# Optimization experiments

Measured on AMD Instinct MI355X. Metric: run time of the kernel, lower is better.

Reference implementation:

```python
import jax, jax.numpy as jnp
import numpy as np

N_NODES = 50000


def setup_inputs() -> dict:
    key = jax.random.key(0)
    k1, k2, k3, k4, k5, k6 = jax.random.split(key, 6)
    c_in, c_out = 64, 64
    n_edges = 800000
    G = jax.random.normal(k1, (N_NODES, c_in), dtype=jnp.float32)
    RSC = jax.random.normal(k2, (N_NODES, c_in), dtype=jnp.float32)
    src = jax.random.randint(k3, (n_edges,), 0, N_NODES, dtype=jnp.int64)
    dst = jax.random.randint(k4, (n_edges,), 0, N_NODES, dtype=jnp.int64)
    W = jax.random.normal(k5, (c_out, c_in), dtype=jnp.float32) / np.sqrt(c_in)
    b = jax.random.normal(k6, (c_out,), dtype=jnp.float32) * 0.01
    return {"G": G, "RSC": RSC, "src": src, "dst": dst, "W": W, "b": b}


def reference(G, RSC, src, dst, W, b):
    # Per-edge relative feature: src node 'G' feature minus dst node 'RSC' feature
    rel = G[src] - RSC[dst]                          # [E, c_in]
    # Linear + ReLU (edge MLP)
    enc = jax.nn.relu(rel @ W.T + b)                 # [E, c_out]
    # Per-dst-node reductions over variable-size mailboxes
    max_agg = jax.ops.segment_max(enc, dst, num_segments=N_NODES)  # -inf for empty
    sum_agg = jax.ops.segment_sum(enc, dst, num_segments=N_NODES)
    cnt = jax.ops.segment_sum(jnp.ones_like(dst, dtype=enc.dtype), dst,
                              num_segments=N_NODES)               # [N]
    has_mail = (cnt > 0)[:, None]
    avg_agg = sum_agg / jnp.maximum(cnt, 1.0)[:, None]
    max_agg = jnp.where(has_mail, max_agg, 0.0)      # nodes w/o edges -> 0
    # concat(max, avg) as in reduce()
    return jnp.concatenate([max_agg, avg_agg], axis=-1)  # [N, 2*c_out]
```

## Files before the change

kernel.cpp:

```cpp
#include <hip/hip_runtime.h>
#include <hip/hip_bf16.h>

#define NCH 64
#define SPAN 64
#define HIST_BLOCKS 256
#define HIST_THREADS 1024
#define NBIN 256
#define NGEMM 768
#define FUSE_THREADS 512
#define NB_CAP 1536

__global__ void detect_init_kernel(const unsigned short* __restrict__ gp, int n16,
                                   const unsigned* __restrict__ ip, int niw,
                                   unsigned* __restrict__ flags,
                                   unsigned* __restrict__ gcnt, int nb) {
    if (blockIdx.x == 0) {
        __shared__ unsigned se, so;
        if (threadIdx.x == 0) { se = 0u; so = 0u; }
        __syncthreads();
        unsigned le = 0u, lo = 0u;
        for (int i = threadIdx.x; i < n16; i += blockDim.x) {
            unsigned ex = (unsigned)((gp[i] >> 7) & 0xFFu);
            if (ex >= 0xC0u) le++;
        }
        for (int i = threadIdx.x; i < niw; i += blockDim.x) {
            if ((i & 1) && ip[i] != 0u) lo++;
        }
        atomicAdd(&se, le);
        atomicAdd(&so, lo);
        __syncthreads();
        if (threadIdx.x == 0) {
            flags[0] = (se > 50u) ? 1u : 0u;
            flags[1] = (so < 50u) ? 1u : 0u;
        }
    } else {
        const int stride = (gridDim.x - 1) * blockDim.x;
        for (int i = (blockIdx.x - 1) * blockDim.x + threadIdx.x; i < nb; i += stride)
            gcnt[i] = 0u;
    }
}

__global__ void bucket_hist_kernel(const void* __restrict__ dstp,
                                   unsigned* __restrict__ gcnt,
                                   const unsigned* __restrict__ flags,
                                   int n_edges, int nb) {
    extern __shared__ unsigned lcnt[];
    for (int i = threadIdx.x; i < nb; i += blockDim.x) lcnt[i] = 0u;
    __syncthreads();
    const unsigned i64 = flags[1];
    const int stride = gridDim.x * blockDim.x;
    for (int e = blockIdx.x * blockDim.x + threadIdx.x; e < n_edges; e += stride) {
        int d = i64 ? (int)((const long long*)dstp)[e] : ((const int*)dstp)[e];
        atomicAdd(&lcnt[d >> 6], 1u);
    }
    __syncthreads();
    for (int i = threadIdx.x; i < nb; i += blockDim.x)
        if (lcnt[i]) atomicAdd(&gcnt[i], lcnt[i]);
}

__global__ void bucket_scan_kernel(const unsigned* __restrict__ gcnt,
                                   unsigned* __restrict__ boffs,
                                   unsigned* __restrict__ cursor, int nb) {
    __shared__ unsigned s[1024];
    const int t = threadIdx.x;
    const int L = (nb + 1023) / 1024;
    unsigned local = 0u;
    for (int i = 0; i < L; ++i) {
        int idx = t * L + i;
        if (idx < nb) local += gcnt[idx];
    }
    s[t] = local;
    __syncthreads();
    for (int off = 1; off < 1024; off <<= 1) {
        unsigned v = (t >= off) ? s[t - off] : 0u;
        __syncthreads();
        s[t] += v;
        __syncthreads();
    }
    unsigned run = s[t] - local;
    for (int i = 0; i < L; ++i) {
        int idx = t * L + i;
        if (idx < nb) { boffs[idx] = run; cursor[idx] = run; run += gcnt[idx]; }
    }
}

__global__ __launch_bounds__(FUSE_THREADS, 4)
void binning_gemm_kernel(const void* __restrict__ srcp, const void* __restrict__ dstp,
                         unsigned* __restrict__ cursor, unsigned* __restrict__ binned,
                         const unsigned* __restrict__ flags, int n_edges, int nb,
                         int depth,
                         const void* __restrict__ Gp, const void* __restrict__ Rp,
                         const void* __restrict__ Wp, const void* __restrict__ bp,
                         void* __restrict__ PQ, int n_nodes) {
    extern __shared__ unsigned lds[];
    if (blockIdx.x < NBIN) {
        unsigned* lcnt = lds;
        unsigned* stage = lds + nb;
        for (int i = threadIdx.x; i < nb; i += blockDim.x) lcnt[i] = 0u;
        __syncthreads();
        const unsigned i64 = flags[1];
        const int chunk = (n_edges + NBIN - 1) / NBIN;
        const int e0 = blockIdx.x * chunk;
        const int e1 = min(e0 + chunk, n_edges);
        for (int e = e0 + threadIdx.x; e < e1; e += blockDim.x) {
            int s, d;
            if (i64) {
                s = (int)((const long long*)srcp)[e];
                d = (int)((const long long*)dstp)[e];
            } else {
                s = ((const int*)srcp)[e];
                d = ((const int*)dstp)[e];
            }
            const int bkt = d >> 6;
            const unsigned pk = ((unsigned)(d & 63) << 26) | (unsigned)s;
            unsigned pos = atomicAdd(&lcnt[bkt], 1u);
            if ((int)pos < depth) {
                stage[bkt * depth + (int)pos] = pk;
            } else {
                unsigned g = atomicAdd(&cursor[bkt], 1u);
                binned[g] = pk;
            }
        }
        __syncthreads();
        for (int bkt = threadIdx.x; bkt < nb; bkt += blockDim.x) {
            int k = min((int)lcnt[bkt], depth);
            if (k > 0) {
                unsigned base = atomicAdd(&cursor[bkt], (unsigned)k);
                for (int i = 0; i < k; ++i) binned[base + i] = stage[bkt * depth + i];
            }
        }
    } else {
        const unsigned f32 = flags[0];
        const int lane = threadIdx.x & 63;
        const int waveInBlk = threadIdx.x >> 6;
        const int wavesPerBlk = blockDim.x >> 6;
        const int gwave = (blockIdx.x - NBIN) * wavesPerBlk + waveInBlk;
        const int nwaves = NGEMM * wavesPerBlk;
        const int n_rows = 2 * n_nodes;
        const int ngroups = (n_rows + 3) / 4;

        float* ldsb = (float*)lds;
        float* slot = &ldsb[waveInBlk * 4 * NCH];

        float w[NCH];
        float bias;
        if (f32) {
            const float* Wf = (const float*)Wp;
            #pragma unroll
            for (int k = 0; k < NCH; ++k) w[k] = Wf[lane * NCH + k];
            bias = ((const float*)bp)[lane];
        } else {
            const __hip_bfloat16* Wh = (const __hip_bfloat16*)Wp;
            #pragma unroll
            for (int k = 0; k < NCH; ++k) w[k] = __bfloat162float(Wh[lane * NCH + k]);
            bias = __bfloat162float(((const __hip_bfloat16*)bp)[lane]);
        }

        const int niter = (ngroups + nwaves - 1) / nwaves;
        for (int it = 0; it < niter; ++it) {
            const int grp = gwave + it * nwaves;
            const bool gvalid = (grp < ngroups);
            const int m0 = grp * 4;
            if (gvalid) {
                const int myrow = m0 + (lane >> 4);
                const int col = (lane & 15) * 4;
                float x0 = 0.f, x1 = 0.f, x2 = 0.f, x3 = 0.f;
                if (myrow < n_rows) {
                    const bool isQ = (myrow >= n_nodes);
                    const int r = isQ ? (myrow - n_nodes) : myrow;
                    const void* inp = isQ ? Rp : Gp;
                    if (f32) {
                        float4 v = *(const float4*)((const float*)inp +
                                                    (size_t)r * NCH + col);
                        x0 = v.x; x1 = v.y; x2 = v.z; x3 = v.w;
                    } else {
                        ushort4 v = *(const ushort4*)((const unsigned short*)inp +
                                                      (size_t)r * NCH + col);
                        x0 = __bfloat162float(*(__hip_bfloat16*)&v.x);
                        x1 = __bfloat162float(*(__hip_bfloat16*)&v.y);
                        x2 = __bfloat162float(*(__hip_bfloat16*)&v.z);
                        x3 = __bfloat162float(*(__hip_bfloat16*)&v.w);
                    }
                }
                const int sb = (lane >> 4) * NCH + col;
                slot[sb + 0] = x0; slot[sb + 1] = x1;
                slot[sb + 2] = x2; slot[sb + 3] = x3;
            }
            __syncthreads();
            if (gvalid) {
                #pragma unroll
                for (int rr = 0; rr < 4; ++rr) {
                    const int m = m0 + rr;
                    if (m < n_rows) {
                        float a0 = 0.f, a1 = 0.f, a2 = 0.f, a3 = 0.f;
                        const float4* r4 = (const float4*)(slot + rr * NCH);
                        #pragma unroll
                        for (int q = 0; q < 16; ++q) {
                            float4 rv = r4[q];
                            a0 = fmaf(rv.x, w[4 * q + 0], a0);
                            a1 = fmaf(rv.y, w[4 * q + 1], a1);
                            a2 = fmaf(rv.z, w[4 * q + 2], a2);
                            a3 = fmaf(rv.w, w[4 * q + 3], a3);
                        }
                        float acc = (a0 + a1) + (a2 + a3);
                        if (m >= n_nodes) acc -= bias;
                        if (f32) ((float*)PQ)[(size_t)m * NCH + lane] = acc;
                        else ((__hip_bfloat16*)PQ)[(size_t)m * NCH + lane] =
                                 __float2bfloat16(acc);
                    }
                }
            }
            __syncthreads();
        }
    }
}

__global__ __launch_bounds__(512)
void bucket_node_kernel(const unsigned* __restrict__ binned,
                        const unsigned* __restrict__ boffs,
                        const unsigned* __restrict__ gcnt,
                        const void* __restrict__ PQ,
                        const unsigned* __restrict__ flags,
                        void* __restrict__ outp, int n_nodes) {
    __shared__ unsigned scnt[SPAN];
    __shared__ unsigned soff[SPAN];
    __shared__ unsigned cur[SPAN];
    __shared__ unsigned dext[SPAN];
    __shared__ unsigned stage[NB_CAP];
    __shared__ unsigned sorted[NB_CAP];

    const int b = blockIdx.x;
    const int tid = threadIdx.x;
    const int estart = (int)boffs[b];
    const int count = (int)gcnt[b];
    const int lim = (count < NB_CAP) ? count : NB_CAP;

    if (tid < SPAN) { scnt[tid] = 0u; dext[tid] = 0u; }
    __syncthreads();

    for (int i = tid; i < count; i += 512) {
        const unsigned pk = binned[estart + i];
        if (i < NB_CAP) { stage[i] = pk; atomicAdd(&scnt[pk >> 26], 1u); }
        else atomicAdd(&dext[pk >> 26], 1u);
    }
    __syncthreads();

    if (tid == 0) {
        unsigned run = 0u;
        #pragma unroll
        for (int i = 0; i < SPAN; ++i) { soff[i] = run; cur[i] = run; run += scnt[i]; }
    }
    __syncthreads();

    for (int i = tid; i < lim; i += 512) {
        const unsigned pk = stage[i];
        const unsigned pos = atomicAdd(&cur[pk >> 26], 1u);
        sorted[pos] = pk & 0x03FFFFFFu;
    }
    __syncthreads();

    const unsigned f32 = flags[0];
    const int lane = tid & 63;
    const int wid = tid >> 6;
    const float* Pf = (const float*)PQ;
    const unsigned short* Ph = (const unsigned short*)PQ;

    for (int nn = wid; nn < SPAN; nn += 8) {
        const int n = b * SPAN + nn;
        if (n >= n_nodes) break;
        float q;
        if (f32) q = Pf[(size_t)(n_nodes + n) * NCH + lane];
        else {
            unsigned short h = Ph[(size_t)(n_nodes + n) * NCH + lane];
            q = __bfloat162float(*(__hip_bfloat16*)&h);
        }
        const int s0i = (int)soff[nn];
        const int scn = (int)scnt[nn];
        float vmax = 0.0f, vsum = 0.0f;
        int j = 0;
        for (; j + 4 <= scn; j += 4) {
            const int e0 = (int)sorted[s0i + j];
            const int e1 = (int)sorted[s0i + j + 1];
            const int e2 = (int)sorted[s0i + j + 2];
            const int e3 = (int)sorted[s0i + j + 3];
            float p0, p1, p2, p3;
            if (f32) {
                p0 = Pf[(size_t)e0 * NCH + lane];
                p1 = Pf[(size_t)e1 * NCH + lane];
                p2 = Pf[(size_t)e2 * NCH + lane];
                p3 = Pf[(size_t)e3 * NCH + lane];
            } else {
                unsigned short h0 = Ph[(size_t)e0 * NCH + lane];
                unsigned short h1 = Ph[(size_t)e1 * NCH + lane];
                unsigned short h2 = Ph[(size_t)e2 * NCH + lane];
                unsigned short h3 = Ph[(size_t)e3 * NCH + lane];
                p0 = __bfloat162float(*(__hip_bfloat16*)&h0);
                p1 = __bfloat162float(*(__hip_bfloat16*)&h1);
                p2 = __bfloat162float(*(__hip_bfloat16*)&h2);
                p3 = __bfloat162float(*(__hip_bfloat16*)&h3);
            }
            const float v0 = fmaxf(p0 - q, 0.0f);
            const float v1 = fmaxf(p1 - q, 0.0f);
            const float v2 = fmaxf(p2 - q, 0.0f);
            const float v3 = fmaxf(p3 - q, 0.0f);
            vmax = fmaxf(fmaxf(vmax, v0), fmaxf(v1, fmaxf(v2, v3)));
            vsum += (v0 + v1) + (v2 + v3);
        }
        for (; j < scn; ++j) {
            const int e = (int)sorted[s0i + j];
            float p;
            if (f32) p = Pf[(size_t)e * NCH + lane];
            else {
                unsigned short h = Ph[(size_t)e * NCH + lane];
                p = __bfloat162float(*(__hip_bfloat16*)&h);
            }
            const float v = fmaxf(p - q, 0.0f);
            vmax = fmaxf(vmax, v);
            vsum += v;
        }
        for (int i = NB_CAP; i < count; ++i) {
            const unsigned pk = binned[estart + i];
            if ((int)(pk >> 26) == nn) {
                const int e = (int)(pk & 0x03FFFFFFu);
                float p;
                if (f32) p = Pf[(size_t)e * NCH + lane];
                else {
                    unsigned short h = Ph[(size_t)e * NCH + lane];
                    p = __bfloat162float(*(__hip_bfloat16*)&h);
                }
                const float v = fmaxf(p - q, 0.0f);
                vmax = fmaxf(vmax, v);
                vsum += v;
            }
        }
        const int deg = scn + (int)dext[nn];
        const float avg = vsum / (float)(deg > 0 ? deg : 1);
        if (f32) {
            float* out = (float*)outp;
            out[(size_t)n * 2 * NCH + lane] = vmax;
            out[(size_t)n * 2 * NCH + NCH + lane] = avg;
        } else {
            __hip_bfloat16* out = (__hip_bfloat16*)outp;
            out[(size_t)n * 2 * NCH + lane] = __float2bfloat16(vmax);
            out[(size_t)n * 2 * NCH + NCH + lane] = __float2bfloat16(avg);
        }
    }
}

extern "C" void kernel_launch(void* const* d_in, const int* in_sizes, int n_in,
                              void* d_out, int out_size, void* d_ws, size_t ws_size,
                              hipStream_t stream) {
    const void* G = d_in[0];
    const void* RSC = d_in[1];
    const void* src = d_in[2];
    const void* dst = d_in[3];
    const void* W = d_in[4];
    const void* b = d_in[5];

    const int n_nodes = in_sizes[0] / NCH;
    const int n_edges = in_sizes[2];
    const int nb = (n_nodes + SPAN - 1) / SPAN;

    char* ws = (char*)d_ws;
    unsigned* flags = (unsigned*)ws;
    size_t off = 256;
    unsigned* binned = (unsigned*)(ws + off);
    off += (((size_t)n_edges * 4 + 255) / 256) * 256;
    unsigned* boffs = (unsigned*)(ws + off);
    off += (((size_t)nb * 4 + 255) / 256) * 256;
    unsigned* cursor = (unsigned*)(ws + off);
    off += (((size_t)nb * 4 + 255) / 256) * 256;
    unsigned* gcnt = (unsigned*)(ws + off);
    off += (((size_t)nb * 4 + 255) / 256) * 256;
    void* PQ = (void*)(ws + off);

    const int n_g_probe = (in_sizes[0] < 8192) ? in_sizes[0] : 8192;
    const int n_idx_probe = (n_edges < 8192) ? n_edges : 8192;

    detect_init_kernel<<<64, 256, 0, stream>>>((const unsigned short*)G, n_g_probe,
                                               (const unsigned*)src, n_idx_probe,
                                               flags, gcnt, nb);

    bucket_hist_kernel<<<HIST_BLOCKS, HIST_THREADS, (size_t)nb * 4, stream>>>(
        dst, gcnt, flags, n_edges, nb);

    bucket_scan_kernel<<<1, 1024, 0, stream>>>(gcnt, boffs, cursor, nb);

    int depth = 9728 / nb - 1;
    if (depth > 19) depth = 19;
    if (depth < 4) depth = 4;
    size_t bin_lds = (size_t)nb * (depth + 1) * 4;
    const size_t gemm_lds = (size_t)(FUSE_THREADS / 64) * 4 * NCH * 4;
    if (bin_lds < gemm_lds) bin_lds = gemm_lds;

    binning_gemm_kernel<<<NBIN + NGEMM, FUSE_THREADS, bin_lds, stream>>>(
        src, dst, cursor, binned, flags, n_edges, nb, depth,
        G, RSC, W, b, PQ, n_nodes);

    bucket_node_kernel<<<nb, 512, 0, stream>>>(binned, boffs, gcnt, PQ, flags,
                                               d_out, n_nodes);
}
```

Baseline: 184.3 us.

## Merge init, histogram, GEMM, scan and binning into one cooperative kernel

Replaces four separate kernel launches (detect/init, histogram, scan, binning+GEMM) with a single cooperative mega-kernel that uses grid-wide syncs between phases. The histogram now overlaps with the node-projection GEMM in the same phase, and binning runs on the whole grid afterwards. The goal is to remove launch gaps and tail idle time between small kernels. The cost is grid-sync overhead, a grid capped at 512 blocks, and a scan that runs on one block while the rest of the grid waits. A phased multi-launch fallback is kept for devices without cooperative launch.

```diff
diff --git a/kernel.cpp b/kernel.cpp
--- a/kernel.cpp
+++ b/kernel.cpp
@@ -1,108 +1,200 @@
 #include <hip/hip_runtime.h>
 #include <hip/hip_bf16.h>
+#include <hip/hip_cooperative_groups.h>
+
+namespace cg = cooperative_groups;
 
 #define NCH 64
 #define SPAN 64
-#define HIST_BLOCKS 256
-#define HIST_THREADS 1024
-#define NBIN 256
-#define NGEMM 768
-#define FUSE_THREADS 512
+#define MEGA_THREADS 512
 #define NB_CAP 1536
 
-__global__ void detect_init_kernel(const unsigned short* __restrict__ gp, int n16,
-                                   const unsigned* __restrict__ ip, int niw,
-                                   unsigned* __restrict__ flags,
-                                   unsigned* __restrict__ gcnt, int nb) {
-    if (blockIdx.x == 0) {
-        __shared__ unsigned se, so;
-        if (threadIdx.x == 0) { se = 0u; so = 0u; }
-        __syncthreads();
-        unsigned le = 0u, lo = 0u;
-        for (int i = threadIdx.x; i < n16; i += blockDim.x) {
-            unsigned ex = (unsigned)((gp[i] >> 7) & 0xFFu);
-            if (ex >= 0xC0u) le++;
-        }
-        for (int i = threadIdx.x; i < niw; i += blockDim.x) {
-            if ((i & 1) && ip[i] != 0u) lo++;
-        }
-        atomicAdd(&se, le);
-        atomicAdd(&so, lo);
-        __syncthreads();
-        if (threadIdx.x == 0) {
-            flags[0] = (se > 50u) ? 1u : 0u;
-            flags[1] = (so < 50u) ? 1u : 0u;
-        }
-    } else {
-        const int stride = (gridDim.x - 1) * blockDim.x;
-        for (int i = (blockIdx.x - 1) * blockDim.x + threadIdx.x; i < nb; i += stride)
-            gcnt[i] = 0u;
-    }
-}
-
-__global__ void bucket_hist_kernel(const void* __restrict__ dstp,
-                                   unsigned* __restrict__ gcnt,
-                                   const unsigned* __restrict__ flags,
-                                   int n_edges, int nb) {
-    extern __shared__ unsigned lcnt[];
-    for (int i = threadIdx.x; i < nb; i += blockDim.x) lcnt[i] = 0u;
-    __syncthreads();
-    const unsigned i64 = flags[1];
-    const int stride = gridDim.x * blockDim.x;
-    for (int e = blockIdx.x * blockDim.x + threadIdx.x; e < n_edges; e += stride) {
-        int d = i64 ? (int)((const long long*)dstp)[e] : ((const int*)dstp)[e];
-        atomicAdd(&lcnt[d >> 6], 1u);
-    }
-    __syncthreads();
-    for (int i = threadIdx.x; i < nb; i += blockDim.x)
-        if (lcnt[i]) atomicAdd(&gcnt[i], lcnt[i]);
-}
-
-__global__ void bucket_scan_kernel(const unsigned* __restrict__ gcnt,
-                                   unsigned* __restrict__ boffs,
-                                   unsigned* __restrict__ cursor, int nb) {
-    __shared__ unsigned s[1024];
-    const int t = threadIdx.x;
-    const int L = (nb + 1023) / 1024;
-    unsigned local = 0u;
-    for (int i = 0; i < L; ++i) {
-        int idx = t * L + i;
-        if (idx < nb) local += gcnt[idx];
-    }
-    s[t] = local;
-    __syncthreads();
-    for (int off = 1; off < 1024; off <<= 1) {
-        unsigned v = (t >= off) ? s[t - off] : 0u;
-        __syncthreads();
-        s[t] += v;
-        __syncthreads();
-    }
-    unsigned run = s[t] - local;
-    for (int i = 0; i < L; ++i) {
-        int idx = t * L + i;
-        if (idx < nb) { boffs[idx] = run; cursor[idx] = run; run += gcnt[idx]; }
-    }
-}
-
-__global__ __launch_bounds__(FUSE_THREADS, 4)
-void binning_gemm_kernel(const void* __restrict__ srcp, const void* __restrict__ dstp,
-                         unsigned* __restrict__ cursor, unsigned* __restrict__ binned,
-                         const unsigned* __restrict__ flags, int n_edges, int nb,
-                         int depth,
-                         const void* __restrict__ Gp, const void* __restrict__ Rp,
-                         const void* __restrict__ Wp, const void* __restrict__ bp,
-                         void* __restrict__ PQ, int n_nodes) {
+__global__ __launch_bounds__(MEGA_THREADS, 4)
+void mega_kernel(const unsigned short* __restrict__ gp16, int n16,
+                 const unsigned* __restrict__ ipw, int niw,
+                 unsigned* __restrict__ flags,
+                 unsigned* __restrict__ gcnt,
+                 unsigned* __restrict__ boffs,
+                 unsigned* __restrict__ cursor,
+                 unsigned* __restrict__ binned,
+                 const void* __restrict__ srcp, const void* __restrict__ dstp,
+                 const void* __restrict__ Gp, const void* __restrict__ Rp,
+                 const void* __restrict__ Wp, const void* __restrict__ bp,
+                 void* __restrict__ PQ,
+                 int n_nodes, int n_edges, int nb, int depth, int phase) {
     extern __shared__ unsigned lds[];
-    if (blockIdx.x < NBIN) {
+    __shared__ unsigned sdet[2];
+    __shared__ unsigned sscan[MEGA_THREADS];
+
+    const int tid = threadIdx.x;
+    const int bid = blockIdx.x;
+    const bool coop = (phase < 0);
+
+    if (coop || phase == 0) {
+        const int stride = gridDim.x * blockDim.x;
+        for (int i = bid * blockDim.x + tid; i < nb; i += stride) gcnt[i] = 0u;
+        if (bid == 0) {
+            if (tid == 0) { sdet[0] = 0u; sdet[1] = 0u; }
+            __syncthreads();
+            unsigned le = 0u, lo = 0u;
+            for (int i = tid; i < n16; i += blockDim.x) {
+                unsigned ex = (unsigned)((gp16[i] >> 7) & 0xFFu);
+                if (ex >= 0xC0u) le++;
+            }
+            for (int i = tid; i < niw; i += blockDim.x) {
+                if ((i & 1) && ipw[i] != 0u) lo++;
+            }
+            atomicAdd(&sdet[0], le);
+            atomicAdd(&sdet[1], lo);
+            __syncthreads();
+            if (tid == 0) {
+                flags[0] = (sdet[0] > 50u) ? 1u : 0u;
+                flags[1] = (sdet[1] < 50u) ? 1u : 0u;
+            }
+        }
+    }
+    if (coop) cg::this_grid().sync();
+
+    if (coop || phase == 1) {
+        const unsigned i64 = flags[1];
+        const int hb = (int)(gridDim.x >> 2);
+        if (bid < hb) {
+            unsigned* lcnt = lds;
+            for (int i = tid; i < nb; i += blockDim.x) lcnt[i] = 0u;
+            __syncthreads();
+            const int stride = hb * (int)blockDim.x;
+            for (int e = bid * (int)blockDim.x + tid; e < n_edges; e += stride) {
+                int d = i64 ? (int)((const long long*)dstp)[e]
+                            : ((const int*)dstp)[e];
+                atomicAdd(&lcnt[d >> 6], 1u);
+            }
+            __syncthreads();
+            for (int i = tid; i < nb; i += blockDim.x)
+                if (lcnt[i]) atomicAdd(&gcnt[i], lcnt[i]);
+        } else {
+            const unsigned f32 = flags[0];
+            const int lane = tid & 63;
+            const int waveInBlk = tid >> 6;
+            const int gwave = (bid - hb) * 8 + waveInBlk;
+            const int nwaves = ((int)gridDim.x - hb) * 8;
+            const int n_rows = 2 * n_nodes;
+            const int ngroups = (n_rows + 3) / 4;
+
+            float* ldsb = (float*)lds;
+            float* slot = &ldsb[waveInBlk * 4 * NCH];
+
+            float w[NCH];
+            float bias;
+            if (f32) {
+                const float* Wf = (const float*)Wp;
+                #pragma unroll
+                for (int k = 0; k < NCH; ++k) w[k] = Wf[lane * NCH + k];
+                bias = ((const float*)bp)[lane];
+            } else {
+                const __hip_bfloat16* Wh = (const __hip_bfloat16*)Wp;
+                #pragma unroll
+                for (int k = 0; k < NCH; ++k)
+                    w[k] = __bfloat162float(Wh[lane * NCH + k]);
+                bias = __bfloat162float(((const __hip_bfloat16*)bp)[lane]);
+            }
+
+            const int niter = (ngroups + nwaves - 1) / nwaves;
+            for (int it = 0; it < niter; ++it) {
+                const int grp = gwave + it * nwaves;
+                const bool gvalid = (grp < ngroups);
+                const int m0 = grp * 4;
+                if (gvalid) {
+                    const int myrow = m0 + (lane >> 4);
+                    const int col = (lane & 15) * 4;
+                    float x0 = 0.f, x1 = 0.f, x2 = 0.f, x3 = 0.f;
+                    if (myrow < n_rows) {
+                        const bool isQ = (myrow >= n_nodes);
+                        const int r = isQ ? (myrow - n_nodes) : myrow;
+                        const void* inp = isQ ? Rp : Gp;
+                        if (f32) {
+                            float4 v = *(const float4*)((const float*)inp +
+                                                        (size_t)r * NCH + col);
+                            x0 = v.x; x1 = v.y; x2 = v.z; x3 = v.w;
+                        } else {
+                            ushort4 v = *(const ushort4*)(
+                                (const unsigned short*)inp + (size_t)r * NCH + col);
+                            x0 = __bfloat162float(*(__hip_bfloat16*)&v.x);
+                            x1 = __bfloat162float(*(__hip_bfloat16*)&v.y);
+                            x2 = __bfloat162float(*(__hip_bfloat16*)&v.z);
+                            x3 = __bfloat162float(*(__hip_bfloat16*)&v.w);
+                        }
+                    }
+                    const int sb = (lane >> 4) * NCH + col;
+                    slot[sb + 0] = x0; slot[sb + 1] = x1;
+                    slot[sb + 2] = x2; slot[sb + 3] = x3;
+                }
+                __syncthreads();
+                if (gvalid) {
+                    #pragma unroll
+                    for (int rr = 0; rr < 4; ++rr) {
+                        const int m = m0 + rr;
+                        if (m < n_rows) {
+                            float a0 = 0.f, a1 = 0.f, a2 = 0.f, a3 = 0.f;
+                            const float4* r4 = (const float4*)(slot + rr * NCH);
+                            #pragma unroll
+                            for (int q = 0; q < 16; ++q) {
+                                float4 rv = r4[q];
+                                a0 = fmaf(rv.x, w[4 * q + 0], a0);
+                                a1 = fmaf(rv.y, w[4 * q + 1], a1);
+                                a2 = fmaf(rv.z, w[4 * q + 2], a2);
+                                a3 = fmaf(rv.w, w[4 * q + 3], a3);
+                            }
+                            float acc = (a0 + a1) + (a2 + a3);
+                            if (m >= n_nodes) acc -= bias;
+                            if (f32) ((float*)PQ)[(size_t)m * NCH + lane] = acc;
+                            else ((__hip_bfloat16*)PQ)[(size_t)m * NCH + lane] =
+                                     __float2bfloat16(acc);
+                        }
+                    }
+                }
+                __syncthreads();
+            }
+        }
+    }
+    if (coop) cg::this_grid().sync();
+
+    if (coop || phase == 2) {
+        if (bid == 0) {
+            const int L = (nb + MEGA_THREADS - 1) / MEGA_THREADS;
+            unsigned local = 0u;
+            for (int i = 0; i < L; ++i) {
+                int idx = tid * L + i;
+                if (idx < nb) local += gcnt[idx];
+            }
+            sscan[tid] = local;
+            __syncthreads();
+            for (int off = 1; off < MEGA_THREADS; off <<= 1) {
+                unsigned v = (tid >= off) ? sscan[tid - off] : 0u;
+                __syncthreads();
+                sscan[tid] += v;
+                __syncthreads();
+            }
+            unsigned run = sscan[tid] - local;
+            for (int i = 0; i < L; ++i) {
+                int idx = tid * L + i;
+                if (idx < nb) {
+                    boffs[idx] = run; cursor[idx] = run; run += gcnt[idx];
+                }
+            }
+        }
+    }
+    if (coop) cg::this_grid().sync();
+
+    if (coop || phase == 3) {
+        const unsigned i64 = flags[1];
         unsigned* lcnt = lds;
         unsigned* stage = lds + nb;
-        for (int i = threadIdx.x; i < nb; i += blockDim.x) lcnt[i] = 0u;
+        for (int i = tid; i < nb; i += blockDim.x) lcnt[i] = 0u;
         __syncthreads();
-        const unsigned i64 = flags[1];
-        const int chunk = (n_edges + NBIN - 1) / NBIN;
-        const int e0 = blockIdx.x * chunk;
+        const int chunk = (n_edges + (int)gridDim.x - 1) / (int)gridDim.x;
+        const int e0 = bid * chunk;
         const int e1 = min(e0 + chunk, n_edges);
-        for (int e = e0 + threadIdx.x; e < e1; e += blockDim.x) {
+        for (int e = e0 + tid; e < e1; e += blockDim.x) {
             int s, d;
             if (i64) {
                 s = (int)((const long long*)srcp)[e];
@@ -122,95 +214,13 @@
             }
         }
         __syncthreads();
-        for (int bkt = threadIdx.x; bkt < nb; bkt += blockDim.x) {
+        for (int bkt = tid; bkt < nb; bkt += blockDim.x) {
             int k = min((int)lcnt[bkt], depth);
             if (k > 0) {
                 unsigned base = atomicAdd(&cursor[bkt], (unsigned)k);
-                for (int i = 0; i < k; ++i) binned[base + i] = stage[bkt * depth + i];
-            }
-        }
-    } else {
-        const unsigned f32 = flags[0];
-        const int lane = threadIdx.x & 63;
-        const int waveInBlk = threadIdx.x >> 6;
-        const int wavesPerBlk = blockDim.x >> 6;
-        const int gwave = (blockIdx.x - NBIN) * wavesPerBlk + waveInBlk;
-        const int nwaves = NGEMM * wavesPerBlk;
-        const int n_rows = 2 * n_nodes;
-        const int ngroups = (n_rows + 3) / 4;
-
-        float* ldsb = (float*)lds;
-        float* slot = &ldsb[waveInBlk * 4 * NCH];
-
-        float w[NCH];
-        float bias;
-        if (f32) {
-            const float* Wf = (const float*)Wp;
-            #pragma unroll
-            for (int k = 0; k < NCH; ++k) w[k] = Wf[lane * NCH + k];
-            bias = ((const float*)bp)[lane];
-        } else {
-            const __hip_bfloat16* Wh = (const __hip_bfloat16*)Wp;
-            #pragma unroll
-            for (int k = 0; k < NCH; ++k) w[k] = __bfloat162float(Wh[lane * NCH + k]);
-            bias = __bfloat162float(((const __hip_bfloat16*)bp)[lane]);
-        }
-
-        const int niter = (ngroups + nwaves - 1) / nwaves;
-        for (int it = 0; it < niter; ++it) {
-            const int grp = gwave + it * nwaves;
-            const bool gvalid = (grp < ngroups);
-            const int m0 = grp * 4;
-            if (gvalid) {
-                const int myrow = m0 + (lane >> 4);
-                const int col = (lane & 15) * 4;
-                float x0 = 0.f, x1 = 0.f, x2 = 0.f, x3 = 0.f;
-                if (myrow < n_rows) {
-                    const bool isQ = (myrow >= n_nodes);
-                    const int r = isQ ? (myrow - n_nodes) : myrow;
-                    const void* inp = isQ ? Rp : Gp;
-                    if (f32) {
-                        float4 v = *(const float4*)((const float*)inp +
-                                                    (size_t)r * NCH + col);
-                        x0 = v.x; x1 = v.y; x2 = v.z; x3 = v.w;
-                    } else {
-                        ushort4 v = *(const ushort4*)((const unsigned short*)inp +
-                                                      (size_t)r * NCH + col);
-                        x0 = __bfloat162float(*(__hip_bfloat16*)&v.x);
-                        x1 = __bfloat162float(*(__hip_bfloat16*)&v.y);
-                        x2 = __bfloat162float(*(__hip_bfloat16*)&v.z);
-                        x3 = __bfloat162float(*(__hip_bfloat16*)&v.w);
-                    }
-                }
-                const int sb = (lane >> 4) * NCH + col;
-                slot[sb + 0] = x0; slot[sb + 1] = x1;
-                slot[sb + 2] = x2; slot[sb + 3] = x3;
-            }
-            __syncthreads();
-            if (gvalid) {
-                #pragma unroll
-                for (int rr = 0; rr < 4; ++rr) {
-                    const int m = m0 + rr;
-                    if (m < n_rows) {
-                        float a0 = 0.f, a1 = 0.f, a2 = 0.f, a3 = 0.f;
-                        const float4* r4 = (const float4*)(slot + rr * NCH);
-                        #pragma unroll
-                        for (int q = 0; q < 16; ++q) {
-                            float4 rv = r4[q];
-                            a0 = fmaf(rv.x, w[4 * q + 0], a0);
-                            a1 = fmaf(rv.y, w[4 * q + 1], a1);
-                            a2 = fmaf(rv.z, w[4 * q + 2], a2);
-                            a3 = fmaf(rv.w, w[4 * q + 3], a3);
-                        }
-                        float acc = (a0 + a1) + (a2 + a3);
-                        if (m >= n_nodes) acc -= bias;
-                        if (f32) ((float*)PQ)[(size_t)m * NCH + lane] = acc;
-                        else ((__hip_bfloat16*)PQ)[(size_t)m * NCH + lane] =
-                                 __float2bfloat16(acc);
-                    }
-                }
-            }
-            __syncthreads();
+                for (int i = 0; i < k; ++i)
+                    binned[base + i] = stage[bkt * depth + i];
+            }
         }
     }
 }
@@ -374,28 +384,66 @@
     off += (((size_t)nb * 4 + 255) / 256) * 256;
     void* PQ = (void*)(ws + off);
 
-    const int n_g_probe = (in_sizes[0] < 8192) ? in_sizes[0] : 8192;
-    const int n_idx_probe = (n_edges < 8192) ? n_edges : 8192;
-
-    detect_init_kernel<<<64, 256, 0, stream>>>((const unsigned short*)G, n_g_probe,
-                                               (const unsigned*)src, n_idx_probe,
-                                               flags, gcnt, nb);
-
-    bucket_hist_kernel<<<HIST_BLOCKS, HIST_THREADS, (size_t)nb * 4, stream>>>(
-        dst, gcnt, flags, n_edges, nb);
-
-    bucket_scan_kernel<<<1, 1024, 0, stream>>>(gcnt, boffs, cursor, nb);
+    int n_g_probe = (in_sizes[0] < 8192) ? in_sizes[0] : 8192;
+    int n_idx_probe = (n_edges < 8192) ? n_edges : 8192;
 
     int depth = 9728 / nb - 1;
     if (depth > 19) depth = 19;
     if (depth < 4) depth = 4;
-    size_t bin_lds = (size_t)nb * (depth + 1) * 4;
-    const size_t gemm_lds = (size_t)(FUSE_THREADS / 64) * 4 * NCH * 4;
-    if (bin_lds < gemm_lds) bin_lds = gemm_lds;
-
-    binning_gemm_kernel<<<NBIN + NGEMM, FUSE_THREADS, bin_lds, stream>>>(
-        src, dst, cursor, binned, flags, n_edges, nb, depth,
-        G, RSC, W, b, PQ, n_nodes);
+    size_t mega_lds = (size_t)nb * (depth + 1) * 4;
+    const size_t gemm_lds = (size_t)(MEGA_THREADS / 64) * 4 * NCH * 4;
+    if (mega_lds < gemm_lds) mega_lds = gemm_lds;
+
+    const unsigned short* gp16 = (const unsigned short*)G;
+    const unsigned* ipw = (const unsigned*)src;
+
+    int coop_attr = 0, ncu = 0, maxblk = 0, dev = 0;
+    (void)hipGetDevice(&dev);
+    (void)hipDeviceGetAttribute(&coop_attr, hipDeviceAttributeCooperativeLaunch,
+                                dev);
+    (void)hipDeviceGetAttribute(&ncu, hipDeviceAttributeMultiprocessorCount, dev);
+    (void)hipOccupancyMaxActiveBlocksPerMultiprocessor(
+        &maxblk, (const void*)mega_kernel, MEGA_THREADS, mega_lds);
+
+    int phase_all = -1;
+    if (coop_attr && maxblk > 0 && ncu > 0) {
+        int cap = maxblk * ncu;
+        int grid = (cap < 512) ? cap : 512;
+        if (grid >= 8) {
+            if (grid == cap && maxblk > 1) grid = cap - ncu;
+            if (grid < 8) grid = 8;
+            void* args[] = {
+                (void*)&gp16, (void*)&n_g_probe, (void*)&ipw, (void*)&n_idx_probe,
+                (void*)&flags, (void*)&gcnt, (void*)&boffs, (void*)&cursor,
+                (void*)&binned,
+                (void*)&src, (void*)&dst,
+                (void*)&G, (void*)&RSC, (void*)&W, (void*)&b,
+                (void*)&PQ, (void*)&n_nodes, (void*)&n_edges, (void*)&nb,
+                (void*)&depth, (void*)&phase_all
+            };
+            hipError_t err = hipLaunchCooperativeKernel(
+                (const void*)mega_kernel, dim3(grid), dim3(MEGA_THREADS), args,
+                (unsigned)mega_lds, stream);
+            if (err == hipSuccess) {
+                bucket_node_kernel<<<nb, 512, 0, stream>>>(
+                    binned, boffs, gcnt, PQ, flags, d_out, n_nodes);
+                return;
+            }
+        }
+    }
+
+    mega_kernel<<<64, MEGA_THREADS, 0, stream>>>(
+        gp16, n_g_probe, ipw, n_idx_probe, flags, gcnt, boffs, cursor, binned,
+        src, dst, G, RSC, W, b, PQ, n_nodes, n_edges, nb, depth, 0);
+    mega_kernel<<<1024, MEGA_THREADS, mega_lds, stream>>>(
+        gp16, n_g_probe, ipw, n_idx_probe, flags, gcnt, boffs, cursor, binned,
+        src, dst, G, RSC, W, b, PQ, n_nodes, n_edges, nb, depth, 1);
+    mega_kernel<<<1, MEGA_THREADS, 0, stream>>>(
+        gp16, n_g_probe, ipw, n_idx_probe, flags, gcnt, boffs, cursor, binned,
+        src, dst, G, RSC, W, b, PQ, n_nodes, n_edges, nb, depth, 2);
+    mega_kernel<<<512, MEGA_THREADS, mega_lds, stream>>>(
+        gp16, n_g_probe, ipw, n_idx_probe, flags, gcnt, boffs, cursor, binned,
+        src, dst, G, RSC, W, b, PQ, n_nodes, n_edges, nb, depth, 3);
 
     bucket_node_kernel<<<nb, 512, 0, stream>>>(binned, boffs, gcnt, PQ, flags,
                                                d_out, n_nodes);
```

New measurement: 464.1 us. 152% more time.

## Replace histogram+scan bucketing with fixed-capacity buckets and a global overflow list

Applied to the files above, without the earlier changes.

Removes the separate dst histogram pass and the single-block prefix scan. Each bucket now gets a fixed slot region of NB_CAP entries, and bucket counters are incremented directly during binning. Edges past capacity go to a global overflow buffer that every node thread scans linearly. This saves two launches and one full pass over dst. The cost is a larger workspace, and a serial overflow scan that would become expensive if buckets overflow often, which is unlikely with uniform random dst (about 1024 edges per bucket).

```diff
diff --git a/kernel.cpp b/kernel.cpp
--- a/kernel.cpp
+++ b/kernel.cpp
@@ -3,8 +3,6 @@
 
 #define NCH 64
 #define SPAN 64
-#define HIST_BLOCKS 256
-#define HIST_THREADS 1024
 #define NBIN 256
 #define NGEMM 768
 #define FUSE_THREADS 512
@@ -16,7 +14,7 @@
                                    unsigned* __restrict__ gcnt, int nb) {
     if (blockIdx.x == 0) {
         __shared__ unsigned se, so;
-        if (threadIdx.x == 0) { se = 0u; so = 0u; }
+        if (threadIdx.x == 0) { se = 0u; so = 0u; flags[2] = 0u; }
         __syncthreads();
         unsigned le = 0u, lo = 0u;
         for (int i = threadIdx.x; i < n16; i += blockDim.x) {
@@ -40,54 +38,11 @@
     }
 }
 
-__global__ void bucket_hist_kernel(const void* __restrict__ dstp,
-                                   unsigned* __restrict__ gcnt,
-                                   const unsigned* __restrict__ flags,
-                                   int n_edges, int nb) {
-    extern __shared__ unsigned lcnt[];
-    for (int i = threadIdx.x; i < nb; i += blockDim.x) lcnt[i] = 0u;
-    __syncthreads();
-    const unsigned i64 = flags[1];
-    const int stride = gridDim.x * blockDim.x;
-    for (int e = blockIdx.x * blockDim.x + threadIdx.x; e < n_edges; e += stride) {
-        int d = i64 ? (int)((const long long*)dstp)[e] : ((const int*)dstp)[e];
-        atomicAdd(&lcnt[d >> 6], 1u);
-    }
-    __syncthreads();
-    for (int i = threadIdx.x; i < nb; i += blockDim.x)
-        if (lcnt[i]) atomicAdd(&gcnt[i], lcnt[i]);
-}
-
-__global__ void bucket_scan_kernel(const unsigned* __restrict__ gcnt,
-                                   unsigned* __restrict__ boffs,
-                                   unsigned* __restrict__ cursor, int nb) {
-    __shared__ unsigned s[1024];
-    const int t = threadIdx.x;
-    const int L = (nb + 1023) / 1024;
-    unsigned local = 0u;
-    for (int i = 0; i < L; ++i) {
-        int idx = t * L + i;
-        if (idx < nb) local += gcnt[idx];
-    }
-    s[t] = local;
-    __syncthreads();
-    for (int off = 1; off < 1024; off <<= 1) {
-        unsigned v = (t >= off) ? s[t - off] : 0u;
-        __syncthreads();
-        s[t] += v;
-        __syncthreads();
-    }
-    unsigned run = s[t] - local;
-    for (int i = 0; i < L; ++i) {
-        int idx = t * L + i;
-        if (idx < nb) { boffs[idx] = run; cursor[idx] = run; run += gcnt[idx]; }
-    }
-}
-
 __global__ __launch_bounds__(FUSE_THREADS, 4)
 void binning_gemm_kernel(const void* __restrict__ srcp, const void* __restrict__ dstp,
-                         unsigned* __restrict__ cursor, unsigned* __restrict__ binned,
-                         const unsigned* __restrict__ flags, int n_edges, int nb,
+                         unsigned* __restrict__ gcnt, unsigned* __restrict__ binned,
+                         unsigned long long* __restrict__ ovbuf,
+                         unsigned* __restrict__ flags, int n_edges, int nb,
                          int depth,
                          const void* __restrict__ Gp, const void* __restrict__ Rp,
                          const void* __restrict__ Wp, const void* __restrict__ bp,
@@ -117,25 +72,41 @@
             if ((int)pos < depth) {
                 stage[bkt * depth + (int)pos] = pk;
             } else {
-                unsigned g = atomicAdd(&cursor[bkt], 1u);
-                binned[g] = pk;
+                unsigned g = atomicAdd(&gcnt[bkt], 1u);
+                if (g < NB_CAP) {
+                    binned[bkt * NB_CAP + g] = pk;
+                } else {
+                    unsigned oi = atomicAdd(&flags[2], 1u);
+                    ovbuf[oi] = ((unsigned long long)(unsigned)d << 32) |
+                                (unsigned long long)(unsigned)s;
+                }
             }
         }
         __syncthreads();
         for (int bkt = threadIdx.x; bkt < nb; bkt += blockDim.x) {
             int k = min((int)lcnt[bkt], depth);
             if (k > 0) {
-                unsigned base = atomicAdd(&cursor[bkt], (unsigned)k);
-                for (int i = 0; i < k; ++i) binned[base + i] = stage[bkt * depth + i];
+                unsigned base = atomicAdd(&gcnt[bkt], (unsigned)k);
+                for (int i = 0; i < k; ++i) {
+                    const unsigned pk = stage[bkt * depth + i];
+                    const unsigned pos = base + (unsigned)i;
+                    if (pos < NB_CAP) {
+                        binned[bkt * NB_CAP + pos] = pk;
+                    } else {
+                        const unsigned d = (unsigned)(bkt * SPAN) + (pk >> 26);
+                        unsigned oi = atomicAdd(&flags[2], 1u);
+                        ovbuf[oi] = ((unsigned long long)d << 32) |
+                                    (unsigned long long)(pk & 0x03FFFFFFu);
+                    }
+                }
             }
         }
     } else {
         const unsigned f32 = flags[0];
         const int lane = threadIdx.x & 63;
         const int waveInBlk = threadIdx.x >> 6;
-        const int wavesPerBlk = blockDim.x >> 6;
-        const int gwave = (blockIdx.x - NBIN) * wavesPerBlk + waveInBlk;
-        const int nwaves = NGEMM * wavesPerBlk;
+        const int gwave = (blockIdx.x - NBIN) * 8 + waveInBlk;
+        const int nwaves = NGEMM * 8;
         const int n_rows = 2 * n_nodes;
         const int ngroups = (n_rows + 3) / 4;
 
@@ -217,31 +188,31 @@
 
 __global__ __launch_bounds__(512)
 void bucket_node_kernel(const unsigned* __restrict__ binned,
-                        const unsigned* __restrict__ boffs,
                         const unsigned* __restrict__ gcnt,
+                        const unsigned long long* __restrict__ ovbuf,
                         const void* __restrict__ PQ,
                         const unsigned* __restrict__ flags,
                         void* __restrict__ outp, int n_nodes) {
     __shared__ unsigned scnt[SPAN];
     __shared__ unsigned soff[SPAN];
     __shared__ unsigned cur[SPAN];
-    __shared__ unsigned dext[SPAN];
     __shared__ unsigned stage[NB_CAP];
     __shared__ unsigned sorted[NB_CAP];
 
     const int b = blockIdx.x;
     const int tid = threadIdx.x;
-    const int estart = (int)boffs[b];
-    const int count = (int)gcnt[b];
-    const int lim = (count < NB_CAP) ? count : NB_CAP;
-
-    if (tid < SPAN) { scnt[tid] = 0u; dext[tid] = 0u; }
+    const int estart = b * NB_CAP;
+    const int gc = (int)gcnt[b];
+    const int count = (gc < NB_CAP) ? gc : NB_CAP;
+    const int n_ov = (int)flags[2];
+
+    if (tid < SPAN) scnt[tid] = 0u;
     __syncthreads();
 
     for (int i = tid; i < count; i += 512) {
         const unsigned pk = binned[estart + i];
-        if (i < NB_CAP) { stage[i] = pk; atomicAdd(&scnt[pk >> 26], 1u); }
-        else atomicAdd(&dext[pk >> 26], 1u);
+        stage[i] = pk;
+        atomicAdd(&scnt[pk >> 26], 1u);
     }
     __syncthreads();
 
@@ -252,7 +223,7 @@
     }
     __syncthreads();
 
-    for (int i = tid; i < lim; i += 512) {
+    for (int i = tid; i < count; i += 512) {
         const unsigned pk = stage[i];
         const unsigned pos = atomicAdd(&cur[pk >> 26], 1u);
         sorted[pos] = pk & 0x03FFFFFFu;
@@ -318,10 +289,12 @@
             vmax = fmaxf(vmax, v);
             vsum += v;
         }
-        for (int i = NB_CAP; i < count; ++i) {
-            const unsigned pk = binned[estart + i];
-            if ((int)(pk >> 26) == nn) {
-                const int e = (int)(pk & 0x03FFFFFFu);
+        int ext = 0;
+        for (int i = 0; i < n_ov; ++i) {
+            const unsigned long long ov = ovbuf[i];
+            const int d = (int)(ov >> 32);
+            if (d == n) {
+                const int e = (int)(ov & 0x03FFFFFFu);
                 float p;
                 if (f32) p = Pf[(size_t)e * NCH + lane];
                 else {
@@ -331,9 +304,10 @@
                 const float v = fmaxf(p - q, 0.0f);
                 vmax = fmaxf(vmax, v);
                 vsum += v;
-            }
-        }
-        const int deg = scn + (int)dext[nn];
+                ext++;
+            }
+        }
+        const int deg = scn + ext;
         const float avg = vsum / (float)(deg > 0 ? deg : 1);
         if (f32) {
             float* out = (float*)outp;
@@ -365,11 +339,9 @@
     unsigned* flags = (unsigned*)ws;
     size_t off = 256;
     unsigned* binned = (unsigned*)(ws + off);
-    off += (((size_t)n_edges * 4 + 255) / 256) * 256;
-    unsigned* boffs = (unsigned*)(ws + off);
-    off += (((size_t)nb * 4 + 255) / 256) * 256;
-    unsigned* cursor = (unsigned*)(ws + off);
-    off += (((size_t)nb * 4 + 255) / 256) * 256;
+    off += (((size_t)nb * NB_CAP * 4 + 255) / 256) * 256;
+    unsigned long long* ovbuf = (unsigned long long*)(ws + off);
+    off += (((size_t)n_edges * 8 + 255) / 256) * 256;
     unsigned* gcnt = (unsigned*)(ws + off);
     off += (((size_t)nb * 4 + 255) / 256) * 256;
     void* PQ = (void*)(ws + off);
@@ -380,11 +352,6 @@
     detect_init_kernel<<<64, 256, 0, stream>>>((const unsigned short*)G, n_g_probe,
                                                (const unsigned*)src, n_idx_probe,
                                                flags, gcnt, nb);
-
-    bucket_hist_kernel<<<HIST_BLOCKS, HIST_THREADS, (size_t)nb * 4, stream>>>(
-        dst, gcnt, flags, n_edges, nb);
-
-    bucket_scan_kernel<<<1, 1024, 0, stream>>>(gcnt, boffs, cursor, nb);
 
     int depth = 9728 / nb - 1;
     if (depth > 19) depth = 19;
@@ -394,9 +361,9 @@
     if (bin_lds < gemm_lds) bin_lds = gemm_lds;
 
     binning_gemm_kernel<<<NBIN + NGEMM, FUSE_THREADS, bin_lds, stream>>>(
-        src, dst, cursor, binned, flags, n_edges, nb, depth,
+        src, dst, gcnt, binned, ovbuf, flags, n_edges, nb, depth,
         G, RSC, W, b, PQ, n_nodes);
 
-    bucket_node_kernel<<<nb, 512, 0, stream>>>(binned, boffs, gcnt, PQ, flags,
+    bucket_node_kernel<<<nb, 512, 0, stream>>>(binned, gcnt, ovbuf, PQ, flags,
                                                d_out, n_nodes);
 }
```

Result: faster. 179.0 us (-2.8%).
